# Performance work log

Measured on AMD Instinct MI355X. Metric: run time of the kernel, lower is better.

## Reference

```python
import jax, jax.numpy as jnp
import numpy as np

B, H, T, D = 2, 16, 2048, 64
R1, R2 = 4, 8


def setup_inputs() -> dict:
    key = jax.random.key(0)
    ks = jax.random.split(key, 7)
    return {
        "q": jax.random.normal(ks[0], (B, H, T, D), dtype=jnp.float32),
        "k": jax.random.normal(ks[1], (B, H, T, D), dtype=jnp.float32),
        "v": jax.random.normal(ks[2], (B, H, T, D), dtype=jnp.float32),
        "W_q": jax.random.normal(ks[3], (H, D, R1 * R2), dtype=jnp.float32) / np.sqrt(D),
        "W_k": jax.random.normal(ks[4], (H, D, R1 * R2), dtype=jnp.float32) / np.sqrt(D),
        "core1": jax.random.normal(ks[5], (H, R1), dtype=jnp.float32),
        "core2": jax.random.normal(ks[6], (H, R2), dtype=jnp.float32),
    }


def reference(q, k, v, W_q, W_k, core1, core2):
    """Kronecker low-rank (LSR) causal attention.

    scores[b,h,m,n] = (1/sqrt(R1*R2)) * sum_r kron[h,r] * (q@W_q)[b,h,m,r] * (k@W_k)[b,h,n,r]
    where kron[h] = core1[h] (x) core2[h]  (per-head Kronecker product).
    """
    Hh, r1 = core1.shape
    r2 = core2.shape[1]
    # per-head Kronecker core vector: (H, R1*R2)
    kron = (core1[:, :, None] * core2[:, None, :]).reshape(Hh, r1 * r2)
    scale = 1.0 / jnp.sqrt(jnp.float32(r1 * r2))
    # low-rank projections, rank R = R1*R2
    q_lr = jnp.einsum("bhtd,hdr->bhtr", q, W_q) * kron[None, :, None, :]  # [B,H,T,R]
    k_lr = jnp.einsum("bhtd,hdr->bhtr", k, W_k)                            # [B,H,T,R]
    scores = jnp.einsum("bhmr,bhnr->bhmn", q_lr, k_lr) * scale             # [B,H,T,T]
    t = q.shape[2]
    causal = jnp.tril(jnp.ones((t, t), dtype=bool))
    scores = jnp.where(causal[None, None], scores, -jnp.inf)
    p = jax.nn.softmax(scores, axis=-1)
    return jnp.einsum("bhmn,bhnd->bhmd", p, v)
```

## Files before the change

kernel.cpp:

```cpp
#include <hip/hip_runtime.h>

typedef _Float16 f16;
typedef _Float16 f16x2 __attribute__((ext_vector_type(2)));
typedef _Float16 f16x4 __attribute__((ext_vector_type(4)));
typedef _Float16 f16x8 __attribute__((ext_vector_type(8)));
typedef float    f32x4 __attribute__((ext_vector_type(4)));
typedef float    f32x16 __attribute__((ext_vector_type(16)));

constexpr int B_ = 2, H_ = 16, T_ = 2048, D_ = 64, R_ = 32, NT = 32;
constexpr int NROW = B_ * H_ * T_;

__device__ __forceinline__ f32x4 mfma16(f16x8 a, f16x8 b, f32x4 c) {
  return __builtin_amdgcn_mfma_f32_16x16x32_f16(a, b, c, 0, 0, 0);
}
__device__ __forceinline__ f32x16 mfma32(f16x8 a, f16x8 b, f32x16 c) {
  return __builtin_amdgcn_mfma_f32_32x32x16_f16(a, b, c, 0, 0, 0);
}
__device__ __forceinline__ void ld_lds16(const void* g, void* l) {
  __builtin_amdgcn_global_load_lds(
      (const __attribute__((address_space(1))) unsigned int*)g,
      (__attribute__((address_space(3))) unsigned int*)l, 16, 0, 0);
}

__global__ __launch_bounds__(256) void proj_kernel(
    const float* __restrict__ q, const float* __restrict__ k, const float* __restrict__ v,
    const float* __restrict__ Wq, const float* __restrict__ Wk,
    const float* __restrict__ c1, const float* __restrict__ c2,
    f16* __restrict__ qlr, f16* __restrict__ klr, f16* __restrict__ vt)
{
  __shared__ f16   sv[64 * 65];
  __shared__ float sW[2][64 * 33];
  __shared__ f16   sO[2][64 * 40];

  const int tid = threadIdx.x, w = tid >> 6, lane = tid & 63;
  const int l15 = lane & 15, l4 = lane >> 4;
  const int bh = blockIdx.x >> 5, h = bh & (H_ - 1);
  const int t0 = (blockIdx.x & 31) * 64;

  const float* vb = v + ((size_t)bh * T_ + t0) * D_;
  float4 vld[4];
#pragma unroll
  for (int it = 0; it < 4; ++it) vld[it] = ((const float4*)vb)[it * 256 + tid];

  const int m = t0 + 16 * w + l15;
  const float* qr = q + ((size_t)bh * T_ + m) * D_;
  const float* kr = k + ((size_t)bh * T_ + m) * D_;
  f16x8 aq[2], ak[2];
#pragma unroll
  for (int kc = 0; kc < 2; ++kc) {
    float4 x0 = *(const float4*)(qr + kc * 32 + 8 * l4);
    float4 x1 = *(const float4*)(qr + kc * 32 + 8 * l4 + 4);
    float4 y0 = *(const float4*)(kr + kc * 32 + 8 * l4);
    float4 y1 = *(const float4*)(kr + kc * 32 + 8 * l4 + 4);
    f16x8 A, K;
    A[0]=(f16)x0.x; A[1]=(f16)x0.y; A[2]=(f16)x0.z; A[3]=(f16)x0.w;
    A[4]=(f16)x1.x; A[5]=(f16)x1.y; A[6]=(f16)x1.z; A[7]=(f16)x1.w;
    K[0]=(f16)y0.x; K[1]=(f16)y0.y; K[2]=(f16)y0.z; K[3]=(f16)y0.w;
    K[4]=(f16)y1.x; K[5]=(f16)y1.y; K[6]=(f16)y1.z; K[7]=(f16)y1.w;
    aq[kc] = A; ak[kc] = K;
  }
  const float* Wqh = Wq + (size_t)h * D_ * R_;
  const float* Wkh = Wk + (size_t)h * D_ * R_;
  float4 wq0 = ((const float4*)Wqh)[tid * 2], wq1 = ((const float4*)Wqh)[tid * 2 + 1];
  float4 wk0 = ((const float4*)Wkh)[tid * 2], wk1 = ((const float4*)Wkh)[tid * 2 + 1];

#pragma unroll
  for (int it = 0; it < 4; ++it) {
    const int i4 = it * 256 + tid, t = i4 >> 4, dq = (i4 & 15) * 4;
    sv[t * 65 + dq    ] = (f16)vld[it].x;
    sv[t * 65 + dq + 1] = (f16)vld[it].y;
    sv[t * 65 + dq + 2] = (f16)vld[it].z;
    sv[t * 65 + dq + 3] = (f16)vld[it].w;
  }
  {
    const int d = tid >> 2, r0 = (tid & 3) * 8;
    float* pq = &sW[0][d * 33 + r0];
    float* pk = &sW[1][d * 33 + r0];
    pq[0]=wq0.x; pq[1]=wq0.y; pq[2]=wq0.z; pq[3]=wq0.w;
    pq[4]=wq1.x; pq[5]=wq1.y; pq[6]=wq1.z; pq[7]=wq1.w;
    pk[0]=wk0.x; pk[1]=wk0.y; pk[2]=wk0.z; pk[3]=wk0.w;
    pk[4]=wk1.x; pk[5]=wk1.y; pk[6]=wk1.z; pk[7]=wk1.w;
  }
  __syncthreads();

  const f32x4 z4 = {0.f, 0.f, 0.f, 0.f};
#pragma unroll
  for (int nt = 0; nt < 2; ++nt) {
    const int r = 16 * nt + l15;
    f16x8 bq[2], bk[2];
#pragma unroll
    for (int kc = 0; kc < 2; ++kc)
#pragma unroll
      for (int j2 = 0; j2 < 8; ++j2) {
        const int d = kc * 32 + 8 * l4 + j2;
        bq[kc][j2] = (f16)sW[0][d * 33 + r];
        bk[kc][j2] = (f16)sW[1][d * 33 + r];
      }
    f32x4 accq = mfma16(aq[0], bq[0], z4); accq = mfma16(aq[1], bq[1], accq);
    f32x4 acck = mfma16(ak[0], bk[0], z4); acck = mfma16(ak[1], bk[1], acck);
    const float scl = c1[h * 4 + (r >> 3)] * c2[h * 8 + (r & 7)] *
                      (0.17677669529663687f * 1.4426950408889634f);
#pragma unroll
    for (int i = 0; i < 4; ++i) {
      const int row = 16 * w + 4 * l4 + i;
      sO[0][row * 40 + r] = (f16)(accq[i] * scl);
      sO[1][row * 40 + r] = (f16)acck[i];
    }
  }
  __syncthreads();

  {
    const int row = tid >> 2, seg = (tid & 3) * 8;
    const size_t g = ((size_t)bh * T_ + t0 + row) * R_ + seg;
    *(f16x8*)(qlr + g) = *(const f16x8*)&sO[0][row * 40 + seg];
    *(f16x8*)(klr + g) = *(const f16x8*)&sO[1][row * 40 + seg];
  }
#pragma unroll
  for (int it = 0; it < 8; ++it) {
    const int idx = it * 256 + tid, d = idx >> 5, t = (idx & 31) * 2;
    f16x2 pr; pr[0] = sv[t * 65 + d]; pr[1] = sv[(t + 1) * 65 + d];
    const int sw = ((((t >> 3) ^ (d & 7)) << 3) | (t & 7));
    *(f16x2*)(vt + ((size_t)bh * D_ + d) * T_ + t0 + sw) = pr;
  }
}

__global__ __launch_bounds__(128) void attn_kernel(
    const f16* __restrict__ qlr, const f16* __restrict__ klr,
    const f16* __restrict__ vt, f16* __restrict__ On, float2* __restrict__ ml,
    const int ns_shift)
{
  __shared__ __align__(16) f16 s_k[64 * 32];
  __shared__ __align__(16) f16 s_vt[64 * 64];
  __shared__ __align__(16) f16 s_p[2][32 * 64];

  const int tid = threadIdx.x, w = tid >> 6, lane = tid & 63;
  const int l15 = lane & 15, l4 = lane >> 4, l31 = lane & 31, hh = lane >> 5;
  const int NS = 1 << ns_shift;
  const int bh = blockIdx.x & 31;
  const int rest = blockIdx.x >> 5;
  const int mt = 31 - (rest >> ns_shift);
  const int s  = rest & (NS - 1);
  const int m0 = mt * 64;

  const f16x8 aq0 = *(const f16x8*)(qlr + ((size_t)bh * T_ + m0 + 32 * w + l15) * R_ + 8 * l4);
  const f16x8 aq1 = *(const f16x8*)(qlr + ((size_t)bh * T_ + m0 + 32 * w + 16 + l15) * R_ + 8 * l4);

  const f16* kb = klr + (size_t)bh * T_ * R_;
  const f16* vb = vt + (size_t)bh * D_ * T_;

  f32x16 oacc[2];
#pragma unroll
  for (int c = 0; c < 2; ++c)
#pragma unroll
    for (int e = 0; e < 16; ++e) oacc[c][e] = 0.f;
  float mi0 = -1e30f, mi1 = -1e30f, li0 = 0.f, li1 = 0.f;
  const f32x4 z4 = {0.f, 0.f, 0.f, 0.f};

  for (int j = s; j <= mt; j += NS) {
    const int n0 = 64 * j;
    __syncthreads();
#pragma unroll
    for (int e = 0; e < 2; ++e)
      ld_lds16((const char*)kb + (size_t)n0 * 64 + (2 * w + e) * 1024 + lane * 16,
               (char*)s_k + (2 * w + e) * 1024);
#pragma unroll
    for (int e = 0; e < 4; ++e) {
      const int d0 = w * 32 + e * 8;
      ld_lds16((const char*)vb + ((size_t)(d0 + (lane >> 3)) * T_ + n0) * 2 + (lane & 7) * 16,
               (char*)s_vt + d0 * 128);
    }
    __syncthreads();

    f32x4 sc[4][2];
#pragma unroll
    for (int ns = 0; ns < 4; ++ns) {
      f16x8 akf = *(const f16x8*)&s_k[(16 * ns + l15) * 32 + 8 * l4];
      sc[ns][0] = mfma16(akf, aq0, z4);
      sc[ns][1] = mfma16(akf, aq1, z4);
    }
    if (j == mt) {
      const int lim0 = 32 * w + l15;
#pragma unroll
      for (int ns = 0; ns < 4; ++ns) {
        const int nb = 16 * ns + 4 * l4;
#pragma unroll
        for (int i = 0; i < 4; ++i) {
          if (nb + i > lim0)      sc[ns][0][i] = -1e30f;
          if (nb + i > lim0 + 16) sc[ns][1][i] = -1e30f;
        }
      }
    }

    float rm0 = -1e30f, rm1 = -1e30f;
#pragma unroll
    for (int ns = 0; ns < 4; ++ns)
#pragma unroll
      for (int i = 0; i < 4; ++i) {
        rm0 = fmaxf(rm0, sc[ns][0][i]);
        rm1 = fmaxf(rm1, sc[ns][1][i]);
      }
    rm0 = fmaxf(rm0, __shfl_xor(rm0, 16)); rm0 = fmaxf(rm0, __shfl_xor(rm0, 32));
    rm1 = fmaxf(rm1, __shfl_xor(rm1, 16)); rm1 = fmaxf(rm1, __shfl_xor(rm1, 32));
    const float mn0 = fmaxf(mi0, rm0), mn1 = fmaxf(mi1, rm1);
    const float a0 = exp2f(mi0 - mn0), a1 = exp2f(mi1 - mn1);
    float rs0 = 0.f, rs1 = 0.f;
#pragma unroll
    for (int ns = 0; ns < 4; ++ns) {
      f16x4 p0v, p1v;
#pragma unroll
      for (int i = 0; i < 4; ++i) {
        const float p0 = exp2f(sc[ns][0][i] - mn0);
        const float p1 = exp2f(sc[ns][1][i] - mn1);
        rs0 += p0; rs1 += p1;
        p0v[i] = (f16)p0; p1v[i] = (f16)p1;
      }
      const int col = ((((2 * ns + (l4 >> 1)) ^ (l15 & 7)) << 3) | (4 * (l4 & 1)));
      *(f16x4*)&s_p[w][l15 * 64 + col]        = p0v;
      *(f16x4*)&s_p[w][(16 + l15) * 64 + col] = p1v;
    }
    rs0 += __shfl_xor(rs0, 16); rs0 += __shfl_xor(rs0, 32);
    rs1 += __shfl_xor(rs1, 16); rs1 += __shfl_xor(rs1, 32);
    li0 = li0 * a0 + rs0; li1 = li1 * a1 + rs1;
    mi0 = mn0; mi1 = mn1;
    const float aPV = (lane & 16) ? a1 : a0;
#pragma unroll
    for (int c = 0; c < 2; ++c) oacc[c] *= aPV;

#pragma unroll
    for (int kc = 0; kc < 4; ++kc) {
      const int u = (2 * kc + hh) ^ (l31 & 7);
      f16x8 bp = *(const f16x8*)&s_p[w][l31 * 64 + u * 8];
#pragma unroll
      for (int c = 0; c < 2; ++c) {
        f16x8 av = *(const f16x8*)&s_vt[(32 * c + l31) * 64 + u * 8];
        oacc[c] = mfma32(av, bp, oacc[c]);
      }
    }
  }

  const float myl = (lane & 16) ? li1 : li0;
  const float invl = myl > 0.f ? 1.f / myl : 0.f;
  f16* ob = On + (((size_t)s * 32 + bh) * T_ + m0 + 32 * w + l31) * D_;
#pragma unroll
  for (int c = 0; c < 2; ++c)
#pragma unroll
    for (int g = 0; g < 4; ++g) {
      f16x4 o;
#pragma unroll
      for (int e = 0; e < 4; ++e) o[e] = (f16)(oacc[c][4 * g + e] * invl);
      *(f16x4*)(ob + 32 * c + 8 * g + 4 * hh) = o;
    }
  if (l4 < 2) {
    float2 mlv;
    mlv.x = l4 ? mi1 : mi0;
    mlv.y = l4 ? li1 : li0;
    ml[((size_t)s * 32 + bh) * T_ + m0 + 32 * w + 16 * l4 + l15] = mlv;
  }
}

__global__ __launch_bounds__(256) void merge_kernel(
    const f16* __restrict__ On, const float2* __restrict__ ml,
    float* __restrict__ out, const int NS)
{
  const int row = blockIdx.x * 32 + (threadIdx.x >> 3);
  const int d0 = (threadIdx.x & 7) * 8;
  float res[8];
  if (NS == 1) {
    const f16x8 o0 = *(const f16x8*)(On + (size_t)row * 64 + d0);
#pragma unroll
    for (int e = 0; e < 8; ++e) res[e] = (float)o0[e];
  } else {
    float2 mls[4];
    float ms = -3e38f;
    for (int s = 0; s < NS; ++s) {
      mls[s] = ml[(size_t)s * NROW + row];
      ms = fmaxf(ms, mls[s].x);
    }
    float wt[4], wsum = 0.f;
    for (int s = 0; s < NS; ++s) {
      wt[s] = exp2f(mls[s].x - ms) * mls[s].y;
      wsum += wt[s];
    }
    const float inv = 1.f / wsum;
#pragma unroll
    for (int e = 0; e < 8; ++e) res[e] = 0.f;
    for (int s = 0; s < NS; ++s) {
      const f16x8 o = *(const f16x8*)(On + ((size_t)s * NROW + row) * 64 + d0);
      const float c = wt[s] * inv;
#pragma unroll
      for (int e = 0; e < 8; ++e) res[e] += c * (float)o[e];
    }
  }
  float* ob = out + (size_t)row * 64 + d0;
  f32x4 r0, r1;
#pragma unroll
  for (int e = 0; e < 4; ++e) { r0[e] = res[e]; r1[e] = res[4 + e]; }
  *(f32x4*)ob = r0;
  *(f32x4*)(ob + 4) = r1;
}

extern "C" void kernel_launch(void* const* d_in, const int* in_sizes, int n_in,
                              void* d_out, int out_size, void* d_ws, size_t ws_size,
                              hipStream_t stream) {
  const float* q  = (const float*)d_in[0];
  const float* k  = (const float*)d_in[1];
  const float* v  = (const float*)d_in[2];
  const float* Wq = (const float*)d_in[3];
  const float* Wk = (const float*)d_in[4];
  const float* c1 = (const float*)d_in[5];
  const float* c2 = (const float*)d_in[6];
  float* out = (float*)d_out;

  f16* qlr = (f16*)d_ws;
  f16* klr = qlr + (size_t)B_ * H_ * T_ * R_;
  f16* vt  = klr + (size_t)B_ * H_ * T_ * R_;
  f16* On  = vt + (size_t)B_ * H_ * T_ * D_;

  const size_t projB = (size_t)16 * 1024 * 1024;
  const size_t perSplit = (size_t)NROW * D_ * 2 + (size_t)NROW * 8;
  int ns_shift = 0;
  if (ws_size >= projB + 4 * perSplit) ns_shift = 2;
  else if (ws_size >= projB + 2 * perSplit) ns_shift = 1;
  const int NS = 1 << ns_shift;
  float2* ml = (float2*)(On + (size_t)NS * NROW * D_);

  proj_kernel<<<B_ * H_ * NT, 256, 0, stream>>>(q, k, v, Wq, Wk, c1, c2, qlr, klr, vt);
  attn_kernel<<<B_ * H_ * NT * NS, 128, 0, stream>>>(qlr, klr, vt, On, ml, ns_shift);
  merge_kernel<<<NROW / 32, 256, 0, stream>>>(On, ml, out, NS);
}
```

Measured before the change: 167.4 us.

## Enlarge attention query tile to 128 rows per block and cap KV split at two

```diff
diff --git a/kernel.cpp b/kernel.cpp
--- a/kernel.cpp
+++ b/kernel.cpp
@@ -9,6 +9,7 @@
 
 constexpr int B_ = 2, H_ = 16, T_ = 2048, D_ = 64, R_ = 32, NT = 32;
 constexpr int NROW = B_ * H_ * T_;
+constexpr int MT128 = T_ / 128;
 
 __device__ __forceinline__ f32x4 mfma16(f16x8 a, f16x8 b, f32x4 c) {
   return __builtin_amdgcn_mfma_f32_16x16x32_f16(a, b, c, 0, 0, 0);
@@ -131,32 +132,39 @@
 {
   __shared__ __align__(16) f16 s_k[64 * 32];
   __shared__ __align__(16) f16 s_vt[64 * 64];
-  __shared__ __align__(16) f16 s_p[2][32 * 64];
+  __shared__ __align__(16) f16 s_p[2][64 * 64];
 
   const int tid = threadIdx.x, w = tid >> 6, lane = tid & 63;
   const int l15 = lane & 15, l4 = lane >> 4, l31 = lane & 31, hh = lane >> 5;
   const int NS = 1 << ns_shift;
   const int bh = blockIdx.x & 31;
   const int rest = blockIdx.x >> 5;
-  const int mt = 31 - (rest >> ns_shift);
+  const int mt = (MT128 - 1) - (rest >> ns_shift);
   const int s  = rest & (NS - 1);
-  const int m0 = mt * 64;
-
-  const f16x8 aq0 = *(const f16x8*)(qlr + ((size_t)bh * T_ + m0 + 32 * w + l15) * R_ + 8 * l4);
-  const f16x8 aq1 = *(const f16x8*)(qlr + ((size_t)bh * T_ + m0 + 32 * w + 16 + l15) * R_ + 8 * l4);
+  const int m0 = mt * 128;
+  const int mw = m0 + 64 * w;
+
+  f16x8 aq[4];
+#pragma unroll
+  for (int msub = 0; msub < 4; ++msub)
+    aq[msub] = *(const f16x8*)(qlr + ((size_t)bh * T_ + mw + 16 * msub + l15) * R_ + 8 * l4);
 
   const f16* kb = klr + (size_t)bh * T_ * R_;
   const f16* vb = vt + (size_t)bh * D_ * T_;
 
-  f32x16 oacc[2];
+  f32x16 oacc[2][2];
 #pragma unroll
   for (int c = 0; c < 2; ++c)
 #pragma unroll
-    for (int e = 0; e < 16; ++e) oacc[c][e] = 0.f;
-  float mi0 = -1e30f, mi1 = -1e30f, li0 = 0.f, li1 = 0.f;
+    for (int mh = 0; mh < 2; ++mh)
+#pragma unroll
+      for (int e = 0; e < 16; ++e) oacc[c][mh][e] = 0.f;
+  float mi[4] = {-1e30f, -1e30f, -1e30f, -1e30f};
+  float li[4] = {0.f, 0.f, 0.f, 0.f};
   const f32x4 z4 = {0.f, 0.f, 0.f, 0.f};
 
-  for (int j = s; j <= mt; j += NS) {
+  const int jmax = 2 * mt + 1;
+  for (int j = s; j <= jmax; j += NS) {
     const int n0 = 64 * j;
     __syncthreads();
 #pragma unroll
@@ -171,90 +179,104 @@
     }
     __syncthreads();
 
-    f32x4 sc[4][2];
-#pragma unroll
-    for (int ns = 0; ns < 4; ++ns) {
-      f16x8 akf = *(const f16x8*)&s_k[(16 * ns + l15) * 32 + 8 * l4];
-      sc[ns][0] = mfma16(akf, aq0, z4);
-      sc[ns][1] = mfma16(akf, aq1, z4);
-    }
-    if (j == mt) {
-      const int lim0 = 32 * w + l15;
+    if (n0 <= mw + 63) {
+      f32x4 sc[4][4];
 #pragma unroll
       for (int ns = 0; ns < 4; ++ns) {
-        const int nb = 16 * ns + 4 * l4;
-#pragma unroll
-        for (int i = 0; i < 4; ++i) {
-          if (nb + i > lim0)      sc[ns][0][i] = -1e30f;
-          if (nb + i > lim0 + 16) sc[ns][1][i] = -1e30f;
+        const f16x8 akf = *(const f16x8*)&s_k[(16 * ns + l15) * 32 + 8 * l4];
+#pragma unroll
+        for (int msub = 0; msub < 4; ++msub)
+          sc[ns][msub] = mfma16(akf, aq[msub], z4);
+      }
+      if (n0 == mw) {
+#pragma unroll
+        for (int ns = 0; ns < 4; ++ns) {
+          const int nb = 16 * ns + 4 * l4;
+#pragma unroll
+          for (int msub = 0; msub < 4; ++msub) {
+            const int lim = 16 * msub + l15;
+#pragma unroll
+            for (int i = 0; i < 4; ++i)
+              if (nb + i > lim) sc[ns][msub][i] = -1e30f;
+          }
         }
       }
-    }
-
-    float rm0 = -1e30f, rm1 = -1e30f;
-#pragma unroll
-    for (int ns = 0; ns < 4; ++ns)
-#pragma unroll
-      for (int i = 0; i < 4; ++i) {
-        rm0 = fmaxf(rm0, sc[ns][0][i]);
-        rm1 = fmaxf(rm1, sc[ns][1][i]);
-      }
-    rm0 = fmaxf(rm0, __shfl_xor(rm0, 16)); rm0 = fmaxf(rm0, __shfl_xor(rm0, 32));
-    rm1 = fmaxf(rm1, __shfl_xor(rm1, 16)); rm1 = fmaxf(rm1, __shfl_xor(rm1, 32));
-    const float mn0 = fmaxf(mi0, rm0), mn1 = fmaxf(mi1, rm1);
-    const float a0 = exp2f(mi0 - mn0), a1 = exp2f(mi1 - mn1);
-    float rs0 = 0.f, rs1 = 0.f;
-#pragma unroll
-    for (int ns = 0; ns < 4; ++ns) {
-      f16x4 p0v, p1v;
-#pragma unroll
-      for (int i = 0; i < 4; ++i) {
-        const float p0 = exp2f(sc[ns][0][i] - mn0);
-        const float p1 = exp2f(sc[ns][1][i] - mn1);
-        rs0 += p0; rs1 += p1;
-        p0v[i] = (f16)p0; p1v[i] = (f16)p1;
-      }
-      const int col = ((((2 * ns + (l4 >> 1)) ^ (l15 & 7)) << 3) | (4 * (l4 & 1)));
-      *(f16x4*)&s_p[w][l15 * 64 + col]        = p0v;
-      *(f16x4*)&s_p[w][(16 + l15) * 64 + col] = p1v;
-    }
-    rs0 += __shfl_xor(rs0, 16); rs0 += __shfl_xor(rs0, 32);
-    rs1 += __shfl_xor(rs1, 16); rs1 += __shfl_xor(rs1, 32);
-    li0 = li0 * a0 + rs0; li1 = li1 * a1 + rs1;
-    mi0 = mn0; mi1 = mn1;
-    const float aPV = (lane & 16) ? a1 : a0;
-#pragma unroll
-    for (int c = 0; c < 2; ++c) oacc[c] *= aPV;
-
-#pragma unroll
-    for (int kc = 0; kc < 4; ++kc) {
-      const int u = (2 * kc + hh) ^ (l31 & 7);
-      f16x8 bp = *(const f16x8*)&s_p[w][l31 * 64 + u * 8];
-#pragma unroll
-      for (int c = 0; c < 2; ++c) {
-        f16x8 av = *(const f16x8*)&s_vt[(32 * c + l31) * 64 + u * 8];
-        oacc[c] = mfma32(av, bp, oacc[c]);
-      }
-    }
-  }
-
-  const float myl = (lane & 16) ? li1 : li0;
-  const float invl = myl > 0.f ? 1.f / myl : 0.f;
-  f16* ob = On + (((size_t)s * 32 + bh) * T_ + m0 + 32 * w + l31) * D_;
-#pragma unroll
-  for (int c = 0; c < 2; ++c)
-#pragma unroll
-    for (int g = 0; g < 4; ++g) {
-      f16x4 o;
-#pragma unroll
-      for (int e = 0; e < 4; ++e) o[e] = (f16)(oacc[c][4 * g + e] * invl);
-      *(f16x4*)(ob + 32 * c + 8 * g + 4 * hh) = o;
-    }
-  if (l4 < 2) {
-    float2 mlv;
-    mlv.x = l4 ? mi1 : mi0;
-    mlv.y = l4 ? li1 : li0;
-    ml[((size_t)s * 32 + bh) * T_ + m0 + 32 * w + 16 * l4 + l15] = mlv;
+
+      float mn[4], al[4], rs[4];
+#pragma unroll
+      for (int msub = 0; msub < 4; ++msub) {
+        float rm = -1e30f;
+#pragma unroll
+        for (int ns = 0; ns < 4; ++ns)
+#pragma unroll
+          for (int i = 0; i < 4; ++i) rm = fmaxf(rm, sc[ns][msub][i]);
+        rm = fmaxf(rm, __shfl_xor(rm, 16)); rm = fmaxf(rm, __shfl_xor(rm, 32));
+        mn[msub] = fmaxf(mi[msub], rm);
+        al[msub] = exp2f(mi[msub] - mn[msub]);
+        rs[msub] = 0.f;
+      }
+#pragma unroll
+      for (int ns = 0; ns < 4; ++ns) {
+        const int col = ((((2 * ns + (l4 >> 1)) ^ (l15 & 7)) << 3) | (4 * (l4 & 1)));
+#pragma unroll
+        for (int msub = 0; msub < 4; ++msub) {
+          f16x4 pv;
+#pragma unroll
+          for (int i = 0; i < 4; ++i) {
+            const float p = exp2f(sc[ns][msub][i] - mn[msub]);
+            rs[msub] += p;
+            pv[i] = (f16)p;
+          }
+          *(f16x4*)&s_p[w][(16 * msub + l15) * 64 + col] = pv;
+        }
+      }
+#pragma unroll
+      for (int msub = 0; msub < 4; ++msub) {
+        rs[msub] += __shfl_xor(rs[msub], 16);
+        rs[msub] += __shfl_xor(rs[msub], 32);
+        li[msub] = li[msub] * al[msub] + rs[msub];
+        mi[msub] = mn[msub];
+      }
+      const float aPV0 = al[l4 & 1];
+      const float aPV1 = al[2 + (l4 & 1)];
+#pragma unroll
+      for (int c = 0; c < 2; ++c) { oacc[c][0] *= aPV0; oacc[c][1] *= aPV1; }
+
+#pragma unroll
+      for (int kc = 0; kc < 4; ++kc) {
+        const int u = (2 * kc + hh) ^ (l31 & 7);
+        const f16x8 bp0 = *(const f16x8*)&s_p[w][l31 * 64 + u * 8];
+        const f16x8 bp1 = *(const f16x8*)&s_p[w][(32 + l31) * 64 + u * 8];
+#pragma unroll
+        for (int c = 0; c < 2; ++c) {
+          const f16x8 av = *(const f16x8*)&s_vt[(32 * c + l31) * 64 + u * 8];
+          oacc[c][0] = mfma32(av, bp0, oacc[c][0]);
+          oacc[c][1] = mfma32(av, bp1, oacc[c][1]);
+        }
+      }
+    }
+  }
+
+#pragma unroll
+  for (int mh = 0; mh < 2; ++mh) {
+    const float myl = li[2 * mh + (l4 & 1)];
+    const float invl = myl > 0.f ? 1.f / myl : 0.f;
+    f16* ob = On + (((size_t)s * 32 + bh) * T_ + mw + 32 * mh + l31) * D_;
+#pragma unroll
+    for (int c = 0; c < 2; ++c)
+#pragma unroll
+      for (int g = 0; g < 4; ++g) {
+        f16x4 o;
+#pragma unroll
+        for (int e = 0; e < 4; ++e) o[e] = (f16)(oacc[c][mh][4 * g + e] * invl);
+        *(f16x4*)(ob + 32 * c + 8 * g + 4 * hh) = o;
+      }
+  }
+  {
+    const float mm = (l4 & 2) ? ((l4 & 1) ? mi[3] : mi[2]) : ((l4 & 1) ? mi[1] : mi[0]);
+    const float ll = (l4 & 2) ? ((l4 & 1) ? li[3] : li[2]) : ((l4 & 1) ? li[1] : li[0]);
+    float2 mlv; mlv.x = mm; mlv.y = ll;
+    ml[((size_t)s * 32 + bh) * T_ + mw + 16 * l4 + l15] = mlv;
   }
 }
 
@@ -319,12 +341,11 @@
   const size_t projB = (size_t)16 * 1024 * 1024;
   const size_t perSplit = (size_t)NROW * D_ * 2 + (size_t)NROW * 8;
   int ns_shift = 0;
-  if (ws_size >= projB + 4 * perSplit) ns_shift = 2;
-  else if (ws_size >= projB + 2 * perSplit) ns_shift = 1;
+  if (ws_size >= projB + 2 * perSplit) ns_shift = 1;
   const int NS = 1 << ns_shift;
   float2* ml = (float2*)(On + (size_t)NS * NROW * D_);
 
   proj_kernel<<<B_ * H_ * NT, 256, 0, stream>>>(q, k, v, Wq, Wk, c1, c2, qlr, klr, vt);
-  attn_kernel<<<B_ * H_ * NT * NS, 128, 0, stream>>>(qlr, klr, vt, On, ml, ns_shift);
+  attn_kernel<<<B_ * H_ * MT128 * NS, 128, 0, stream>>>(qlr, klr, vt, On, ml, ns_shift);
   merge_kernel<<<NROW / 32, 256, 0, stream>>>(On, ml, out, NS);
 }
```

New measurement: 172.9 us. 3.3% more time.

## Drop LDS staging in attention; use MFMA-fragment layouts and register P shuffles

Applied to the files above, without the earlier changes.

```diff
diff --git a/kernel.cpp b/kernel.cpp
--- a/kernel.cpp
+++ b/kernel.cpp
@@ -2,12 +2,13 @@
 
 typedef _Float16 f16;
 typedef _Float16 f16x2 __attribute__((ext_vector_type(2)));
-typedef _Float16 f16x4 __attribute__((ext_vector_type(4)));
 typedef _Float16 f16x8 __attribute__((ext_vector_type(8)));
 typedef float    f32x4 __attribute__((ext_vector_type(4)));
 typedef float    f32x16 __attribute__((ext_vector_type(16)));
+typedef unsigned int u32;
 
 constexpr int B_ = 2, H_ = 16, T_ = 2048, D_ = 64, R_ = 32, NT = 32;
+constexpr int MT = 16;
 constexpr int NROW = B_ * H_ * T_;
 
 __device__ __forceinline__ f32x4 mfma16(f16x8 a, f16x8 b, f32x4 c) {
@@ -16,11 +17,10 @@
 __device__ __forceinline__ f32x16 mfma32(f16x8 a, f16x8 b, f32x16 c) {
   return __builtin_amdgcn_mfma_f32_32x32x16_f16(a, b, c, 0, 0, 0);
 }
-__device__ __forceinline__ void ld_lds16(const void* g, void* l) {
-  __builtin_amdgcn_global_load_lds(
-      (const __attribute__((address_space(1))) unsigned int*)g,
-      (__attribute__((address_space(3))) unsigned int*)l, 16, 0, 0);
-}
+__device__ __forceinline__ u32 pkrtz(float a, float b) {
+  return __builtin_bit_cast(u32, __builtin_amdgcn_cvt_pkrtz(a, b));
+}
+
 
 __global__ __launch_bounds__(256) void proj_kernel(
     const float* __restrict__ q, const float* __restrict__ k, const float* __restrict__ v,
@@ -35,7 +35,7 @@
   const int tid = threadIdx.x, w = tid >> 6, lane = tid & 63;
   const int l15 = lane & 15, l4 = lane >> 4;
   const int bh = blockIdx.x >> 5, h = bh & (H_ - 1);
-  const int t0 = (blockIdx.x & 31) * 64;
+  const int jt = blockIdx.x & 31, t0 = jt * 64;
 
   const float* vb = v + ((size_t)bh * T_ + t0) * D_;
   float4 vld[4];
@@ -110,151 +110,141 @@
   __syncthreads();
 
   {
-    const int row = tid >> 2, seg = (tid & 3) * 8;
-    const size_t g = ((size_t)bh * T_ + t0 + row) * R_ + seg;
-    *(f16x8*)(qlr + g) = *(const f16x8*)&sO[0][row * 40 + seg];
-    *(f16x8*)(klr + g) = *(const f16x8*)&sO[1][row * 40 + seg];
+    const int row = tid >> 2, q4 = tid & 3;
+    const size_t base = ((((size_t)bh * 32 + jt) * 2 + (q4 >> 1)) * 2 + (q4 & 1)) * 64 + row;
+    *(f16x8*)(qlr + base * 8) = *(const f16x8*)&sO[0][row * 40 + q4 * 8];
+    *(f16x8*)(klr + base * 8) = *(const f16x8*)&sO[1][row * 40 + q4 * 8];
   }
 #pragma unroll
   for (int it = 0; it < 8; ++it) {
-    const int idx = it * 256 + tid, d = idx >> 5, t = (idx & 31) * 2;
+    const int d = tid >> 2, i2 = (tid & 3) * 2, t = it * 8 + i2;
     f16x2 pr; pr[0] = sv[t * 65 + d]; pr[1] = sv[(t + 1) * 65 + d];
-    const int sw = ((((t >> 3) ^ (d & 7)) << 3) | (t & 7));
-    *(f16x2*)(vt + ((size_t)bh * D_ + d) * T_ + t0 + sw) = pr;
-  }
-}
-
-__global__ __launch_bounds__(128) void attn_kernel(
+    *(f16x2*)(vt + (((size_t)bh * 32 + jt) * 8 + it) * 512 + d * 8 + i2) = pr;
+  }
+}
+
+__global__ __launch_bounds__(256, 4) void attn_kernel(
     const f16* __restrict__ qlr, const f16* __restrict__ klr,
     const f16* __restrict__ vt, f16* __restrict__ On, float2* __restrict__ ml,
     const int ns_shift)
 {
-  __shared__ __align__(16) f16 s_k[64 * 32];
-  __shared__ __align__(16) f16 s_vt[64 * 64];
-  __shared__ __align__(16) f16 s_p[2][32 * 64];
-
   const int tid = threadIdx.x, w = tid >> 6, lane = tid & 63;
-  const int l15 = lane & 15, l4 = lane >> 4, l31 = lane & 31, hh = lane >> 5;
+  const int l31 = lane & 31, hh = lane >> 5;
   const int NS = 1 << ns_shift;
   const int bh = blockIdx.x & 31;
   const int rest = blockIdx.x >> 5;
-  const int mt = 31 - (rest >> ns_shift);
+  const int mt = (MT - 1) - (rest >> ns_shift);
   const int s  = rest & (NS - 1);
-  const int m0 = mt * 64;
-
-  const f16x8 aq0 = *(const f16x8*)(qlr + ((size_t)bh * T_ + m0 + 32 * w + l15) * R_ + 8 * l4);
-  const f16x8 aq1 = *(const f16x8*)(qlr + ((size_t)bh * T_ + m0 + 32 * w + 16 + l15) * R_ + 8 * l4);
-
-  const f16* kb = klr + (size_t)bh * T_ * R_;
-  const f16* vb = vt + (size_t)bh * D_ * T_;
+  const int mw = mt * 128 + 32 * w;
+
+  const int jm = mw >> 6, mloc = (mw & 63) + l31;
+  const f16* qb = qlr + (((size_t)bh * 32 + jm) * 2048) + hh * 512 + (size_t)mloc * 8;
+  const f16x8 bq0 = *(const f16x8*)(qb);
+  const f16x8 bq1 = *(const f16x8*)(qb + 1024);
+
+  const f16* kb = klr + (size_t)bh * 32 * 2048;
+  const f16* vb = vt + (size_t)bh * 32 * 4096;
 
   f32x16 oacc[2];
-#pragma unroll
-  for (int c = 0; c < 2; ++c)
-#pragma unroll
-    for (int e = 0; e < 16; ++e) oacc[c][e] = 0.f;
-  float mi0 = -1e30f, mi1 = -1e30f, li0 = 0.f, li1 = 0.f;
-  const f32x4 z4 = {0.f, 0.f, 0.f, 0.f};
-
-  for (int j = s; j <= mt; j += NS) {
-    const int n0 = 64 * j;
-    __syncthreads();
-#pragma unroll
-    for (int e = 0; e < 2; ++e)
-      ld_lds16((const char*)kb + (size_t)n0 * 64 + (2 * w + e) * 1024 + lane * 16,
-               (char*)s_k + (2 * w + e) * 1024);
-#pragma unroll
-    for (int e = 0; e < 4; ++e) {
-      const int d0 = w * 32 + e * 8;
-      ld_lds16((const char*)vb + ((size_t)(d0 + (lane >> 3)) * T_ + n0) * 2 + (lane & 7) * 16,
-               (char*)s_vt + d0 * 128);
-    }
-    __syncthreads();
-
-    f32x4 sc[4][2];
-#pragma unroll
-    for (int ns = 0; ns < 4; ++ns) {
-      f16x8 akf = *(const f16x8*)&s_k[(16 * ns + l15) * 32 + 8 * l4];
-      sc[ns][0] = mfma16(akf, aq0, z4);
-      sc[ns][1] = mfma16(akf, aq1, z4);
-    }
-    if (j == mt) {
-      const int lim0 = 32 * w + l15;
-#pragma unroll
-      for (int ns = 0; ns < 4; ++ns) {
-        const int nb = 16 * ns + 4 * l4;
-#pragma unroll
-        for (int i = 0; i < 4; ++i) {
-          if (nb + i > lim0)      sc[ns][0][i] = -1e30f;
-          if (nb + i > lim0 + 16) sc[ns][1][i] = -1e30f;
+  f32x16 z16;
+#pragma unroll
+  for (int e = 0; e < 16; ++e) { z16[e] = 0.f; oacc[0][e] = 0.f; oacc[1][e] = 0.f; }
+  float mi = -1e30f, li = 0.f;
+
+  const int jw = 2 * mt + (w >> 1);
+  for (int j = s; j <= jw; j += NS) {
+    const f16* kj = kb + (size_t)j * 2048;
+    const f16* vj = vb + (size_t)j * 4096;
+
+    f32x16 sc[2];
+#pragma unroll
+    for (int nt = 0; nt < 2; ++nt) {
+      const int nl = 32 * nt + l31;
+      const f16x8 a0 = *(const f16x8*)(kj + hh * 512 + nl * 8);
+      const f16x8 a1 = *(const f16x8*)(kj + 1024 + hh * 512 + nl * 8);
+      sc[nt] = mfma32(a0, bq0, z16);
+      sc[nt] = mfma32(a1, bq1, sc[nt]);
+    }
+    const int n0 = j * 64;
+    if (n0 + 63 > mw) {
+      const int lim = mw + l31 - n0;
+#pragma unroll
+      for (int nt = 0; nt < 2; ++nt)
+#pragma unroll
+        for (int e = 0; e < 16; ++e) {
+          const int nv = 32 * nt + 4 * hh + (e & 3) + 8 * (e >> 2);
+          if (nv > lim) sc[nt][e] = -1e30f;
+        }
+    }
+
+    float rm = -1e30f;
+#pragma unroll
+    for (int nt = 0; nt < 2; ++nt)
+#pragma unroll
+      for (int e = 0; e < 16; ++e) rm = fmaxf(rm, sc[nt][e]);
+    rm = fmaxf(rm, __shfl_xor(rm, 32));
+    const float mn = fmaxf(mi, rm);
+    const float alpha = exp2f(mi - mn);
+    float rs = 0.f;
+    u32 pk[2][8];
+#pragma unroll
+    for (int nt = 0; nt < 2; ++nt)
+#pragma unroll
+      for (int s4 = 0; s4 < 4; ++s4) {
+        const float p0 = exp2f(sc[nt][4 * s4 + 0] - mn);
+        const float p1 = exp2f(sc[nt][4 * s4 + 1] - mn);
+        const float p2 = exp2f(sc[nt][4 * s4 + 2] - mn);
+        const float p3 = exp2f(sc[nt][4 * s4 + 3] - mn);
+        rs += (p0 + p1) + (p2 + p3);
+        pk[nt][2 * s4]     = pkrtz(p0, p1);
+        pk[nt][2 * s4 + 1] = pkrtz(p2, p3);
+      }
+    rs += __shfl_xor(rs, 32);
+    li = li * alpha + rs; mi = mn;
+#pragma unroll
+    for (int c = 0; c < 2; ++c)
+#pragma unroll
+      for (int e = 0; e < 16; ++e) oacc[c][e] *= alpha;
+
+#pragma unroll
+    for (int nt = 0; nt < 2; ++nt)
+#pragma unroll
+      for (int kcp = 0; kcp < 2; ++kcp) {
+        const int kc = 2 * nt + kcp;
+        const u32 sA = hh ? pk[nt][4 * kcp]     : pk[nt][4 * kcp + 2];
+        const u32 sB = hh ? pk[nt][4 * kcp + 1] : pk[nt][4 * kcp + 3];
+        const u32 kA = hh ? pk[nt][4 * kcp + 2] : pk[nt][4 * kcp];
+        const u32 kB = hh ? pk[nt][4 * kcp + 3] : pk[nt][4 * kcp + 1];
+        const u32 r0 = (u32)__shfl_xor((int)sA, 32);
+        const u32 r1 = (u32)__shfl_xor((int)sB, 32);
+        union { f16x8 v; u32 u[4]; } bp;
+        bp.u[0] = hh ? r0 : kA;
+        bp.u[1] = hh ? r1 : kB;
+        bp.u[2] = hh ? kA : r0;
+        bp.u[3] = hh ? kB : r1;
+#pragma unroll
+        for (int c = 0; c < 2; ++c) {
+          const f16x8 av = *(const f16x8*)(vj + (size_t)(kc * 2 + hh) * 512 + (32 * c + l31) * 8);
+          oacc[c] = mfma32(av, bp.v, oacc[c]);
         }
       }
-    }
-
-    float rm0 = -1e30f, rm1 = -1e30f;
-#pragma unroll
-    for (int ns = 0; ns < 4; ++ns)
-#pragma unroll
-      for (int i = 0; i < 4; ++i) {
-        rm0 = fmaxf(rm0, sc[ns][0][i]);
-        rm1 = fmaxf(rm1, sc[ns][1][i]);
-      }
-    rm0 = fmaxf(rm0, __shfl_xor(rm0, 16)); rm0 = fmaxf(rm0, __shfl_xor(rm0, 32));
-    rm1 = fmaxf(rm1, __shfl_xor(rm1, 16)); rm1 = fmaxf(rm1, __shfl_xor(rm1, 32));
-    const float mn0 = fmaxf(mi0, rm0), mn1 = fmaxf(mi1, rm1);
-    const float a0 = exp2f(mi0 - mn0), a1 = exp2f(mi1 - mn1);
-    float rs0 = 0.f, rs1 = 0.f;
-#pragma unroll
-    for (int ns = 0; ns < 4; ++ns) {
-      f16x4 p0v, p1v;
-#pragma unroll
-      for (int i = 0; i < 4; ++i) {
-        const float p0 = exp2f(sc[ns][0][i] - mn0);
-        const float p1 = exp2f(sc[ns][1][i] - mn1);
-        rs0 += p0; rs1 += p1;
-        p0v[i] = (f16)p0; p1v[i] = (f16)p1;
-      }
-      const int col = ((((2 * ns + (l4 >> 1)) ^ (l15 & 7)) << 3) | (4 * (l4 & 1)));
-      *(f16x4*)&s_p[w][l15 * 64 + col]        = p0v;
-      *(f16x4*)&s_p[w][(16 + l15) * 64 + col] = p1v;
-    }
-    rs0 += __shfl_xor(rs0, 16); rs0 += __shfl_xor(rs0, 32);
-    rs1 += __shfl_xor(rs1, 16); rs1 += __shfl_xor(rs1, 32);
-    li0 = li0 * a0 + rs0; li1 = li1 * a1 + rs1;
-    mi0 = mn0; mi1 = mn1;
-    const float aPV = (lane & 16) ? a1 : a0;
-#pragma unroll
-    for (int c = 0; c < 2; ++c) oacc[c] *= aPV;
-
-#pragma unroll
-    for (int kc = 0; kc < 4; ++kc) {
-      const int u = (2 * kc + hh) ^ (l31 & 7);
-      f16x8 bp = *(const f16x8*)&s_p[w][l31 * 64 + u * 8];
-#pragma unroll
-      for (int c = 0; c < 2; ++c) {
-        f16x8 av = *(const f16x8*)&s_vt[(32 * c + l31) * 64 + u * 8];
-        oacc[c] = mfma32(av, bp, oacc[c]);
-      }
-    }
-  }
-
-  const float myl = (lane & 16) ? li1 : li0;
-  const float invl = myl > 0.f ? 1.f / myl : 0.f;
-  f16* ob = On + (((size_t)s * 32 + bh) * T_ + m0 + 32 * w + l31) * D_;
+  }
+
+  const float invl = li > 0.f ? 1.f / li : 0.f;
+  f16* ob = On + (((size_t)s * 32 + bh) * T_ + mw + l31) * D_;
 #pragma unroll
   for (int c = 0; c < 2; ++c)
 #pragma unroll
-    for (int g = 0; g < 4; ++g) {
-      f16x4 o;
-#pragma unroll
-      for (int e = 0; e < 4; ++e) o[e] = (f16)(oacc[c][4 * g + e] * invl);
-      *(f16x4*)(ob + 32 * c + 8 * g + 4 * hh) = o;
-    }
-  if (l4 < 2) {
-    float2 mlv;
-    mlv.x = l4 ? mi1 : mi0;
-    mlv.y = l4 ? li1 : li0;
-    ml[((size_t)s * 32 + bh) * T_ + m0 + 32 * w + 16 * l4 + l15] = mlv;
+    for (int s4 = 0; s4 < 4; ++s4) {
+      const int d0 = 32 * c + 8 * s4 + 4 * hh;
+      const u32 e0 = pkrtz(oacc[c][4 * s4] * invl, oacc[c][4 * s4 + 1] * invl);
+      const u32 e1 = pkrtz(oacc[c][4 * s4 + 2] * invl, oacc[c][4 * s4 + 3] * invl);
+      *(u32*)(ob + d0)     = e0;
+      *(u32*)(ob + d0 + 2) = e1;
+    }
+  if (!hh) {
+    float2 mlv; mlv.x = mi; mlv.y = li;
+    ml[((size_t)s * 32 + bh) * T_ + mw + l31] = mlv;
   }
 }
 
@@ -319,12 +309,11 @@
   const size_t projB = (size_t)16 * 1024 * 1024;
   const size_t perSplit = (size_t)NROW * D_ * 2 + (size_t)NROW * 8;
   int ns_shift = 0;
-  if (ws_size >= projB + 4 * perSplit) ns_shift = 2;
-  else if (ws_size >= projB + 2 * perSplit) ns_shift = 1;
+  if (ws_size >= projB + 2 * perSplit) ns_shift = 1;
   const int NS = 1 << ns_shift;
   float2* ml = (float2*)(On + (size_t)NS * NROW * D_);
 
   proj_kernel<<<B_ * H_ * NT, 256, 0, stream>>>(q, k, v, Wq, Wk, c1, c2, qlr, klr, vt);
-  attn_kernel<<<B_ * H_ * NT * NS, 128, 0, stream>>>(qlr, klr, vt, On, ml, ns_shift);
+  attn_kernel<<<B_ * H_ * MT * NS, 256, 0, stream>>>(qlr, klr, vt, On, ml, ns_shift);
   merge_kernel<<<NROW / 32, 256, 0, stream>>>(On, ml, out, NS);
 }
```

Result: no change. 165.4 us (-1.2%).
